# Performance work log

Measured on AMD Instinct MI355X. Metric: run time of the kernel, lower is better.

Reference implementation:

```python
import jax, jax.numpy as jnp
import numpy as np

B, S, K = 32, 16384, 64  # batch, num_samples, num_clusters


def _neg_idx(num_clusters):
    # Static column indices kept per row by mask_correlated_samples: drop
    # the diagonal and the (i, K+i)/(K+i, i) positive pairs -> N-2 cols/row.
    N = 2 * num_clusters
    idx = []
    for r in range(N):
        partner = r + num_clusters if r < num_clusters else r - num_clusters
        idx.append([c for c in range(N) if c != r and c != partner])
    return np.asarray(idx, dtype=np.int32)  # [N, N-2]


def target_distribution(q):
    # q: [S, K]. weight = q^2 / colsum; then row-normalize.
    w = q ** 2.0 / jnp.sum(q, axis=0)
    return w / jnp.sum(w, axis=1, keepdims=True)


def setup_inputs() -> dict:
    key = jax.random.key(0)
    k1, k2 = jax.random.split(key)
    q_i = jax.random.uniform(k1, (B, S, K), dtype=jnp.float32)
    q_j = jax.random.uniform(k2, (B, S, K), dtype=jnp.float32)
    temperature_l = jnp.asarray(1.0, dtype=jnp.float32)
    return {"q_i": q_i, "q_j": q_j, "temperature_l": temperature_l}


def reference(q_i, q_j, temperature_l):
    num_clusters = q_i.shape[2]
    N = 2 * num_clusters
    neg_idx = jnp.asarray(_neg_idx(num_clusters))  # static, [N, N-2]
    rows = jnp.arange(N)[:, None]

    def per_batch(qi_b, qj_b):
        pi = target_distribution(qi_b).T  # [K, S]
        pj = target_distribution(qj_b).T  # [K, S]
        q = jnp.concatenate([pi, pj], axis=0)        # [N, S]
        sim = jnp.matmul(q, q.T) / temperature_l      # [N, N]
        pos = jnp.concatenate(
            [jnp.diagonal(sim, num_clusters), jnp.diagonal(sim, -num_clusters)]
        )[:, None]                                    # [N, 1]
        neg = sim[rows, neg_idx]                      # [N, N-2]
        logits = jnp.concatenate([pos, neg], axis=1)  # [N, N-1], label = 0
        # CrossEntropyLoss(reduction='sum') with labels all zero
        loss = jnp.sum(jax.nn.logsumexp(logits, axis=1) - logits[:, 0])
        return loss / N

    losses = jax.vmap(per_batch)(q_i, q_j)  # [B]
    return jnp.mean(losses)
```

## Files before the change

kernel.cpp:

```cpp
#include <hip/hip_runtime.h>
#include <math.h>

#define Bn 32
#define Sn 16384
#define Kn 64
#define Nn 128

#define P1  16
#define NSB 32
#define SPB (Sn/NSB)
#define NCH (SPB/32)

typedef __attribute__((ext_vector_type(8))) short bf16x8;
typedef __attribute__((ext_vector_type(4))) float f32x4;

#define WS_CSPART 0
#define WS_GRAM   (Bn*2*P1*64)
#define WS_LOSS   (WS_GRAM + Bn*3*4096)
#define WS_PART   (WS_LOSS + Bn)
#define WS_PART_SZ ((size_t)Bn*NSB*3*4096)

__device__ __forceinline__ unsigned short f2bf(float f) {
    unsigned int u = __float_as_uint(f);
    u += 0x7FFFu + ((u >> 16) & 1u);
    return (unsigned short)(u >> 16);
}

__global__ __launch_bounds__(256) void k_colsum(const float* __restrict__ qi,
                                                const float* __restrict__ qj,
                                                float* __restrict__ ws) {
    const int blk   = blockIdx.x;
    const int chunk = blk % P1;
    const int pair  = blk / P1;
    const int v = pair & 1, b = pair >> 1;
    const float* __restrict__ src = v ? qj : qi;
    const int tid = threadIdx.x;
    const int c4 = (tid & 15) * 4;
    const int sg = tid >> 4;
    const long base = (long)b * Sn * Kn + (long)chunk * (Sn / P1) * Kn;
    const float* __restrict__ p0 = src + base + (long)sg * Kn + c4;

    float4 acc = make_float4(0.f, 0.f, 0.f, 0.f);
    #pragma unroll 1
    for (int g = 0; g < 4; ++g) {
        float4 vv[16];
        #pragma unroll
        for (int u = 0; u < 16; ++u)
            vv[u] = *(const float4*)(p0 + (long)(g * 16 + u) * 16 * Kn);
        #pragma unroll
        for (int u = 0; u < 16; ++u) {
            acc.x += vv[u].x; acc.y += vv[u].y;
            acc.z += vv[u].z; acc.w += vv[u].w;
        }
    }
    __shared__ float red[16 * 64];
    *(float4*)&red[sg * 64 + c4] = acc;
    __syncthreads();
    if (tid < 64) {
        float s = 0.f;
        #pragma unroll
        for (int g = 0; g < 16; ++g) s += red[g * 64 + tid];
        ws[WS_CSPART + (pair * P1 + chunk) * 64 + tid] = s;
    }
}

template<int ATOMIC>
__global__ __launch_bounds__(256, 4) void k_gram(const float* __restrict__ qi,
                                                 const float* __restrict__ qj,
                                                 float* __restrict__ ws) {
    const int b   = blockIdx.x / NSB;
    const int sb  = blockIdx.x % NSB;
    const int tid = threadIdx.x;
    const int w   = tid >> 6;
    const int l   = tid & 63;
    const int lc  = tid & 15;
    const int sp  = tid >> 4;
    const int c0  = lc * 4;

    __shared__ unsigned short lp[2][2][64 * 40];
    __shared__ float csh[128];

    if (tid < 128) {
        const int view = tid >> 6, col = tid & 63;
        float s = 0.f;
        #pragma unroll
        for (int p = 0; p < P1; ++p)
            s += ws[WS_CSPART + ((b * 2 + view) * P1 + p) * 64 + col];
        csh[view * 64 + col] = s;
    }
    __syncthreads();

    const float icI[4] = {1.f / csh[c0], 1.f / csh[c0 + 1],
                          1.f / csh[c0 + 2], 1.f / csh[c0 + 3]};
    const float icJ[4] = {1.f / csh[64 + c0], 1.f / csh[64 + c0 + 1],
                          1.f / csh[64 + c0 + 2], 1.f / csh[64 + c0 + 3]};

    f32x4 aII[4], aIJ[4], aJJ[4];
    #pragma unroll
    for (int t = 0; t < 4; ++t) {
        aII[t] = (f32x4){0.f, 0.f, 0.f, 0.f};
        aIJ[t] = (f32x4){0.f, 0.f, 0.f, 0.f};
        aJJ[t] = (f32x4){0.f, 0.f, 0.f, 0.f};
    }

    const long bb  = (long)b * Sn * Kn;
    const long s0g = (long)sb * SPB;

    float4 pfa[2], pfb[2];

    auto issue = [&](int ct) {
        const long off = bb + (s0g + ct * 32 + 2 * sp) * (long)Kn + c0;
        pfa[0] = *(const float4*)(qi + off);
        pfb[0] = *(const float4*)(qi + off + Kn);
        pfa[1] = *(const float4*)(qj + off);
        pfb[1] = *(const float4*)(qj + off + Kn);
    };
    auto stage = [&](int buf) {
        #pragma unroll
        for (int v = 0; v < 2; ++v) {
            const float* ic = v ? icJ : icI;
            const float4 qa = pfa[v], qb = pfb[v];
            float wa[4] = {qa.x * qa.x * ic[0], qa.y * qa.y * ic[1],
                           qa.z * qa.z * ic[2], qa.w * qa.w * ic[3]};
            float wb[4] = {qb.x * qb.x * ic[0], qb.y * qb.y * ic[1],
                           qb.z * qb.z * ic[2], qb.w * qb.w * ic[3]};
            float ra = wa[0] + wa[1] + wa[2] + wa[3];
            float rb = wb[0] + wb[1] + wb[2] + wb[3];
            #pragma unroll
            for (int d = 1; d < 16; d <<= 1) {
                ra += __shfl_xor(ra, d);
                rb += __shfl_xor(rb, d);
            }
            const float ia = 1.f / ra, ib = 1.f / rb;
            #pragma unroll
            for (int cc = 0; cc < 4; ++cc) {
                const unsigned int pk = (unsigned int)f2bf(wa[cc] * ia)
                                      | ((unsigned int)f2bf(wb[cc] * ib) << 16);
                *(unsigned int*)&lp[buf][v][(c0 + cc) * 40 + 2 * sp] = pk;
            }
        }
    };

    issue(0);
    stage(0);
    issue(1);
    __syncthreads();

    const int sgo = (l >> 4) * 8;
    for (int ct = 0; ct < NCH; ++ct) {
        const int cur = ct & 1;
        const bf16x8 ai = *(const bf16x8*)&lp[cur][0][(w * 16 + lc) * 40 + sgo];
        const bf16x8 aj = *(const bf16x8*)&lp[cur][1][(w * 16 + lc) * 40 + sgo];
        #pragma unroll
        for (int nt = 0; nt < 4; ++nt) {
            const bf16x8 fi = *(const bf16x8*)&lp[cur][0][(nt * 16 + lc) * 40 + sgo];
            const bf16x8 fj = *(const bf16x8*)&lp[cur][1][(nt * 16 + lc) * 40 + sgo];
            aII[nt] = __builtin_amdgcn_mfma_f32_16x16x32_bf16(ai, fi, aII[nt], 0, 0, 0);
            aIJ[nt] = __builtin_amdgcn_mfma_f32_16x16x32_bf16(ai, fj, aIJ[nt], 0, 0, 0);
            aJJ[nt] = __builtin_amdgcn_mfma_f32_16x16x32_bf16(aj, fj, aJJ[nt], 0, 0, 0);
        }
        if (ct + 1 < NCH) {
            stage(cur ^ 1);
            if (ct + 2 < NCH) issue(ct + 2);
        }
        __syncthreads();
    }

    const int row0 = w * 16 + (l >> 4) * 4;
    if (ATOMIC) {
        float* __restrict__ dst = ws + WS_GRAM + (long)b * 3 * 4096;
        #pragma unroll
        for (int nt = 0; nt < 4; ++nt) {
            #pragma unroll
            for (int r = 0; r < 4; ++r) {
                const int e = (row0 + r) * 64 + nt * 16 + lc;
                atomicAdd(&dst[e],        aII[nt][r]);
                atomicAdd(&dst[4096 + e], aIJ[nt][r]);
                atomicAdd(&dst[8192 + e], aJJ[nt][r]);
            }
        }
    } else {
        float* __restrict__ dst = ws + WS_PART + (long)(b * NSB + sb) * 3 * 4096;
        #pragma unroll
        for (int nt = 0; nt < 4; ++nt) {
            #pragma unroll
            for (int r = 0; r < 4; ++r) {
                const int e = (row0 + r) * 64 + nt * 16 + lc;
                dst[e]        = aII[nt][r];
                dst[4096 + e] = aIJ[nt][r];
                dst[8192 + e] = aJJ[nt][r];
            }
        }
    }
}

__global__ __launch_bounds__(256) void k_gram_reduce(float* __restrict__ ws) {
    const int idx = blockIdx.x * 256 + threadIdx.x;
    const int b = idx / (3 * 4096);
    const int e = idx % (3 * 4096);
    float s = 0.f;
    #pragma unroll 8
    for (int p = 0; p < NSB; ++p)
        s += ws[WS_PART + (long)(b * NSB + p) * 3 * 4096 + e];
    ws[WS_GRAM + (long)b * 3 * 4096 + e] = s;
}

__device__ __forceinline__ float sim_entry(const float* __restrict__ g, int r, int c) {
    if (r < 64) return (c < 64) ? g[r * 64 + c] : g[4096 + r * 64 + (c - 64)];
    return (c < 64) ? g[4096 + c * 64 + (r - 64)] : g[8192 + (r - 64) * 64 + (c - 64)];
}

__global__ __launch_bounds__(128) void k_loss(const float* __restrict__ temp,
                                              float* __restrict__ ws) {
    const int b = blockIdx.x;
    const int r = threadIdx.x;
    const float* __restrict__ g = ws + WS_GRAM + (long)b * 3 * 4096;
    const float inv_t = 1.f / temp[0];
    const int p = r ^ 64;

    float m = -1e30f, pos = 0.f;
    for (int c = 0; c < Nn; ++c) {
        if (c == r) continue;
        const float v = sim_entry(g, r, c) * inv_t;
        m = fmaxf(m, v);
        if (c == p) pos = v;
    }
    float sum = 0.f;
    for (int c = 0; c < Nn; ++c) {
        if (c == r) continue;
        const float v = sim_entry(g, r, c) * inv_t;
        sum += expf(v - m);
    }
    const float val = m + logf(sum) - pos;

    __shared__ float red[Nn];
    red[r] = val;
    __syncthreads();
    for (int st = 64; st > 0; st >>= 1) {
        if (r < st) red[r] += red[r + st];
        __syncthreads();
    }
    if (r == 0) ws[WS_LOSS + b] = red[0] / (float)Nn;
}

__global__ void k_final(float* __restrict__ ws, float* __restrict__ out) {
    if (threadIdx.x == 0) {
        float s = 0.f;
        for (int b = 0; b < Bn; ++b) s += ws[WS_LOSS + b];
        out[0] = s / (float)Bn;
    }
}

extern "C" void kernel_launch(void* const* d_in, const int* in_sizes, int n_in,
                              void* d_out, int out_size, void* d_ws, size_t ws_size,
                              hipStream_t stream) {
    const float* qi   = (const float*)d_in[0];
    const float* qj   = (const float*)d_in[1];
    const float* temp = (const float*)d_in[2];
    float* ws  = (float*)d_ws;
    float* out = (float*)d_out;

    const size_t need_f = (size_t)WS_PART + WS_PART_SZ;
    const bool partial = ws_size >= need_f * sizeof(float);

    k_colsum<<<Bn * 2 * P1, 256, 0, stream>>>(qi, qj, ws);

    if (partial) {
        k_gram<0><<<Bn * NSB, 256, 0, stream>>>(qi, qj, ws);
        k_gram_reduce<<<(Bn * 3 * 4096) / 256, 256, 0, stream>>>(ws);
    } else {
        hipMemsetAsync(ws + WS_GRAM, 0, (size_t)Bn * 3 * 4096 * sizeof(float), stream);
        k_gram<1><<<Bn * NSB, 256, 0, stream>>>(qi, qj, ws);
    }

    k_loss<<<Bn, 128, 0, stream>>>(temp, ws);
    k_final<<<1, 64, 0, stream>>>(ws, out);
}
```

Before: 163.4 us.

## Restructure column-sum kernel to read both views per block with double-buffered loads

The column-sum kernel now has each block cover both q_i and q_j for one sample range, using 64 sample chunks per batch instead of 16 chunks per view. Loads are double-buffered across two register sets with barriers between stages, and the access pattern mirrors the gram kernel's sample tiling, which may improve cache locality for the following pass. The gram kernel now sums 64 partials per column instead of 16, adding a small cost at its start. The per-iteration __syncthreads calls and the lower number of loads in flight could limit memory throughput compared with the previous 16-deep unrolled loads.

After: 168.2 us. 3.0% more time.

```diff
diff --git a/kernel.cpp b/kernel.cpp
--- a/kernel.cpp
+++ b/kernel.cpp
@@ -6,7 +6,10 @@
 #define Kn 64
 #define Nn 128
 
-#define P1  16
+#define NSC 64
+#define SPC (Sn/NSC)
+#define NCC (SPC/32)
+
 #define NSB 32
 #define SPB (Sn/NSB)
 #define NCH (SPB/32)
@@ -15,7 +18,7 @@
 typedef __attribute__((ext_vector_type(4))) float f32x4;
 
 #define WS_CSPART 0
-#define WS_GRAM   (Bn*2*P1*64)
+#define WS_GRAM   (Bn*2*NSC*64)
 #define WS_LOSS   (WS_GRAM + Bn*3*4096)
 #define WS_PART   (WS_LOSS + Bn)
 #define WS_PART_SZ ((size_t)Bn*NSB*3*4096)
@@ -29,38 +32,57 @@
 __global__ __launch_bounds__(256) void k_colsum(const float* __restrict__ qi,
                                                 const float* __restrict__ qj,
                                                 float* __restrict__ ws) {
-    const int blk   = blockIdx.x;
-    const int chunk = blk % P1;
-    const int pair  = blk / P1;
-    const int v = pair & 1, b = pair >> 1;
-    const float* __restrict__ src = v ? qj : qi;
+    const int blk = blockIdx.x;
+    const int b   = blk / NSC;
+    const int sb  = blk % NSC;
     const int tid = threadIdx.x;
-    const int c4 = (tid & 15) * 4;
-    const int sg = tid >> 4;
-    const long base = (long)b * Sn * Kn + (long)chunk * (Sn / P1) * Kn;
-    const float* __restrict__ p0 = src + base + (long)sg * Kn + c4;
-
-    float4 acc = make_float4(0.f, 0.f, 0.f, 0.f);
+    const int sp  = tid >> 4;
+    const int c0  = (tid & 15) * 4;
+
+    const long bb = (long)b * Sn * Kn;
+    const long s0 = (long)sb * SPC;
+
+    f32x4 A0, A1, A2, A3, B0, B1, B2, B3;
+
+    auto issueA = [&](int ct) {
+        const long off = bb + (s0 + ct * 32 + 2 * sp) * (long)Kn + c0;
+        A0 = *(const f32x4*)(qi + off);
+        A1 = *(const f32x4*)(qi + off + Kn);
+        A2 = *(const f32x4*)(qj + off);
+        A3 = *(const f32x4*)(qj + off + Kn);
+    };
+    auto issueB = [&](int ct) {
+        const long off = bb + (s0 + ct * 32 + 2 * sp) * (long)Kn + c0;
+        B0 = *(const f32x4*)(qi + off);
+        B1 = *(const f32x4*)(qi + off + Kn);
+        B2 = *(const f32x4*)(qj + off);
+        B3 = *(const f32x4*)(qj + off + Kn);
+    };
+
+    f32x4 aI = {0.f, 0.f, 0.f, 0.f}, aJ = {0.f, 0.f, 0.f, 0.f};
+
+    issueA(0);
+    issueB(1);
     #pragma unroll 1
-    for (int g = 0; g < 4; ++g) {
-        float4 vv[16];
-        #pragma unroll
-        for (int u = 0; u < 16; ++u)
-            vv[u] = *(const float4*)(p0 + (long)(g * 16 + u) * 16 * Kn);
-        #pragma unroll
-        for (int u = 0; u < 16; ++u) {
-            acc.x += vv[u].x; acc.y += vv[u].y;
-            acc.z += vv[u].z; acc.w += vv[u].w;
-        }
-    }
-    __shared__ float red[16 * 64];
-    *(float4*)&red[sg * 64 + c4] = acc;
+    for (int ct = 0; ct < NCC; ct += 2) {
+        aI += A0 + A1; aJ += A2 + A3;
+        if (ct + 2 < NCC) issueA(ct + 2);
+        __syncthreads();
+        aI += B0 + B1; aJ += B2 + B3;
+        if (ct + 3 < NCC) issueB(ct + 3);
+        __syncthreads();
+    }
+
+    __shared__ float red[2][16][64];
+    *(f32x4*)&red[0][sp][c0] = aI;
+    *(f32x4*)&red[1][sp][c0] = aJ;
     __syncthreads();
-    if (tid < 64) {
+    if (tid < 128) {
+        const int view = tid >> 6, col = tid & 63;
         float s = 0.f;
         #pragma unroll
-        for (int g = 0; g < 16; ++g) s += red[g * 64 + tid];
-        ws[WS_CSPART + (pair * P1 + chunk) * 64 + tid] = s;
+        for (int g = 0; g < 16; ++g) s += red[view][g][col];
+        ws[WS_CSPART + ((b * 2 + view) * NSC + sb) * 64 + col] = s;
     }
 }
 
@@ -83,9 +105,9 @@
     if (tid < 128) {
         const int view = tid >> 6, col = tid & 63;
         float s = 0.f;
-        #pragma unroll
-        for (int p = 0; p < P1; ++p)
-            s += ws[WS_CSPART + ((b * 2 + view) * P1 + p) * 64 + col];
+        #pragma unroll 8
+        for (int p = 0; p < NSC; ++p)
+            s += ws[WS_CSPART + ((b * 2 + view) * NSC + p) * 64 + col];
         csh[view * 64 + col] = s;
     }
     __syncthreads();
@@ -263,7 +285,7 @@
     const size_t need_f = (size_t)WS_PART + WS_PART_SZ;
     const bool partial = ws_size >= need_f * sizeof(float);
 
-    k_colsum<<<Bn * 2 * P1, 256, 0, stream>>>(qi, qj, ws);
+    k_colsum<<<Bn * NSC, 256, 0, stream>>>(qi, qj, ws);
 
     if (partial) {
         k_gram<0><<<Bn * NSB, 256, 0, stream>>>(qi, qj, ws);
```
